# Optimization experiments

Hardware: AMD Instinct MI355X
Metric: run time of the kernel (lower is better)

The kernel has to match this reference:

```python
import jax, jax.numpy as jnp
import numpy as np

VOCAB, D, H, NC = 32000, 300, 300, 3
B, S, A, L = 256, 128, 8, 32


def _lstm_dir(x, mask, Wih, Whh, bih, bhh):
    # x: [B,T,D], mask: [B,T] bool. Returns [B,T,H] with padded steps zeroed (like pad_packed_sequence).
    Bn = x.shape[0]
    Hn = Whh.shape[1]

    def step(carry, inp):
        h, c = carry
        xt, mt = inp
        g = xt @ Wih.T + h @ Whh.T + bih + bhh  # [B,4H]
        i, f, gg, o = jnp.split(g, 4, axis=-1)
        i = jax.nn.sigmoid(i)
        f = jax.nn.sigmoid(f)
        o = jax.nn.sigmoid(o)
        cn = f * c + i * jnp.tanh(gg)
        hn = o * jnp.tanh(cn)
        m = mt[:, None]
        h2 = jnp.where(m, hn, h)
        c2 = jnp.where(m, cn, c)
        return (h2, c2), h2 * m

    init = (jnp.zeros((Bn, Hn), x.dtype), jnp.zeros((Bn, Hn), x.dtype))
    _, outs = jax.lax.scan(step, init, (jnp.swapaxes(x, 0, 1), jnp.swapaxes(mask, 0, 1)))
    return jnp.swapaxes(outs, 0, 1)


def _bilstm(x, lengths, Wih_f, Whh_f, bih_f, bhh_f, Wih_b, Whh_b, bih_b, bhh_b):
    # Emulates packed bidirectional LSTM: backward dir runs over the length-aware reversed sequence.
    Tn = x.shape[1]
    t = jnp.arange(Tn)
    mask = t[None, :] < lengths[:, None]
    out_f = _lstm_dir(x, mask, Wih_f, Whh_f, bih_f, bhh_f)
    idx = jnp.clip(lengths[:, None] - 1 - t[None, :], 0, Tn - 1)  # reversal within valid length
    x_rev = jnp.take_along_axis(x, idx[:, :, None], axis=1)
    ob = _lstm_dir(x_rev, mask, Wih_b, Whh_b, bih_b, bhh_b)
    out_b = jnp.take_along_axis(ob, idx[:, :, None], axis=1) * mask[:, :, None]
    return jnp.concatenate([out_f, out_b], axis=-1)  # [B,T,2H]


def setup_inputs() -> dict:
    key = jax.random.key(0)
    ks = jax.random.split(key, 16)
    sc = 0.05
    inp = {
        'text': jax.random.randint(ks[0], (B, S), 1, VOCAB, dtype=jnp.int32),
        'aspect': jax.random.randint(ks[1], (B, A), 1, VOCAB, dtype=jnp.int32),
        'left': jax.random.randint(ks[2], (B, L), 1, VOCAB, dtype=jnp.int32),
        'embedding': jax.random.normal(ks[3], (VOCAB, D), jnp.float32) * sc,
        'Wih_f': jax.random.normal(ks[4], (4 * H, D), jnp.float32) * sc,
        'Whh_f': jax.random.normal(ks[5], (4 * H, H), jnp.float32) * sc,
        'bih_f': jnp.zeros((4 * H,), jnp.float32),
        'bhh_f': jnp.zeros((4 * H,), jnp.float32),
        'Wih_b': jax.random.normal(ks[6], (4 * H, D), jnp.float32) * sc,
        'Whh_b': jax.random.normal(ks[7], (4 * H, H), jnp.float32) * sc,
        'bih_b': jnp.zeros((4 * H,), jnp.float32),
        'bhh_b': jnp.zeros((4 * H,), jnp.float32),
        'w1': jax.random.normal(ks[8], (2 * H, 2 * H), jnp.float32) * sc,
        'w2': jax.random.normal(ks[9], (2 * H, 2 * H), jnp.float32) * sc,
        'fc1_w': jax.random.normal(ks[10], (6 * H,), jnp.float32) * sc,
        'fc1_b': jnp.zeros((), jnp.float32),
        'fc2_w': jax.random.normal(ks[11], (NC, 8 * H), jnp.float32) * sc,
        'fc2_b': jnp.zeros((NC,), jnp.float32),
    }
    return inp


def reference(text, aspect, left, embedding, Wih_f, Whh_f, bih_f, bhh_f,
              Wih_b, Whh_b, bih_b, bhh_b, w1, w2, fc1_w, fc1_b, fc2_w, fc2_b):
    left_len = jnp.sum(left != 0, axis=-1)
    context_len = jnp.sum(text != 0, axis=-1)
    aspect_len = jnp.sum(aspect != 0, axis=-1)

    ctx = embedding[text]  # [B,S,D]
    ctx = _bilstm(ctx, context_len, Wih_f, Whh_f, bih_f, bhh_f, Wih_b, Whh_b, bih_b, bhh_b)  # [B,S,2H]

    # location weighting (locationed_context)
    t = jnp.arange(ctx.shape[1])[None, :].astype(jnp.float32)
    cl = context_len[:, None].astype(jnp.float32)
    ll = left_len[:, None].astype(jnp.float32)
    al = aspect_len[:, None].astype(jnp.float32)
    denom = cl - al + 1.0
    w = jnp.where(t < ll, 1.0 - (ll - t) / denom,
        jnp.where(t < ll + al, 0.0,
        jnp.where(t < cl, 1.0 - (t - ll - al + 1.0) / denom, 0.0)))
    ctx = ctx * w[:, :, None]

    asp = embedding[aspect]  # [B,A,D]
    asp = _bilstm(asp, aspect_len, Wih_f, Whh_f, bih_f, bhh_f, Wih_b, Whh_b, bih_b, bhh_b)  # [B,A,2H]

    # coarse aspect->context
    a_avg = jnp.sum(asp, axis=1) / aspect_len.astype(jnp.float32)[:, None]  # [B,2H]
    s1 = a_avg @ w1
    alpha1 = jax.nn.softmax(jnp.einsum('bd,bsd->bs', s1, ctx), axis=-1)
    mca = jnp.einsum('bs,bsd->bd', alpha1, ctx)

    # coarse context->aspect
    c_avg = jnp.sum(ctx, axis=1) / context_len.astype(jnp.float32)[:, None]
    s2 = c_avg @ w2
    alpha2 = jax.nn.softmax(jnp.einsum('bd,bad->ba', s2, asp), axis=-1)
    mcc = jnp.einsum('ba,bad->bd', alpha2, asp)

    # fine-grained pairwise scores: u[b,s,a] = fc1(cat(ctx_s, asp_a, ctx_s*asp_a))
    # decomposed so the [B,S,A,6H] concat tensor is never materialized
    H2 = ctx.shape[-1]
    wc, wa, wm = fc1_w[:H2], fc1_w[H2:2 * H2], fc1_w[2 * H2:]
    u = (jnp.einsum('bsd,d->bs', ctx, wc)[:, :, None]
         + jnp.einsum('bad,d->ba', asp, wa)[:, None, :]
         + jnp.einsum('bsd,bad->bsa', ctx * wm, asp)
         + fc1_b)  # [B,S,A]

    # fine aspect->context: max over aspect dim, softmax over context positions
    mfa_alpha = jax.nn.softmax(jnp.max(u, axis=2), axis=-1)  # [B,S]
    mfa = jnp.einsum('bs,bsd->bd', mfa_alpha, ctx)

    # fine context->aspect: softmax over aspect dim per position, average-pool over positions
    mfc = jnp.mean(jnp.einsum('bsa,bad->bsd', jax.nn.softmax(u, axis=-1), asp), axis=1)

    m = jnp.concatenate([mca, mcc, mfa, mfc], axis=-1)  # [B,8H]
    return jax.nn.softmax(m @ fc2_w.T + fc2_b, axis=-1)  # [B,NC]
```

## Files before the change

kernel.cpp:

```cpp
#include <hip/hip_runtime.h>
#include <hip/hip_bf16.h>
#include <hip/hip_fp16.h>


#define NB   256
#define NS   128
#define NA   8
#define NL   32
#define ND   300
#define NH   300
#define NPAD  2432
#define TOK_CTX 32768
#define PD    1216
#define HCH   20
#define HSL   4096

typedef _Float16 half8 __attribute__((ext_vector_type(8)));
typedef float    f32x4 __attribute__((ext_vector_type(4)));

__global__ void k_lengths(const int* __restrict__ text, const int* __restrict__ aspect,
                          const int* __restrict__ left, int* __restrict__ lens) {
  int b = threadIdx.x;
  if (b >= NB) return;
  int ll = 0; for (int i = 0; i < NL; i++) ll += (left[b*NL + i] != 0);
  int cl = 0; for (int i = 0; i < NS; i++) cl += (text[b*NS + i] != 0);
  int al = 0; for (int i = 0; i < NA; i++) al += (aspect[b*NA + i] != 0);
  lens[b] = ll; lens[NB + b] = cl; lens[2*NB + b] = al;
}

__global__ void k_cvt_w(const float* __restrict__ Wih_f, const float* __restrict__ Wih_b,
                        const float* __restrict__ Whh_f, const float* __restrict__ Whh_b,
                        const float* __restrict__ bih_f, const float* __restrict__ bhh_f,
                        const float* __restrict__ bih_b, const float* __restrict__ bhh_b,
                        _Float16* __restrict__ Wih_frag, _Float16* __restrict__ Whh_frag,
                        float* __restrict__ bias_sum) {
  int y = blockIdx.y;
  if (y < 2) {
    const float* sf = y ? Whh_f : Wih_f;
    const float* sb = y ? Whh_b : Wih_b;
    _Float16* dst = y ? Whh_frag : Wih_frag;
    const long N = (long)152*10*512;
    for (long i = (long)blockIdx.x*blockDim.x + threadIdx.x; i < N; i += (long)gridDim.x*blockDim.x) {
      long q = i >> 9; int r512 = (int)(i & 511);
      int l = r512 >> 3, e = r512 & 7;
      int k0 = (int)(q % 10);
      int ntile = (int)(q / 10);
      int n = ntile*16 + (l & 15);
      int k = k0*32 + (l >> 4)*8 + e;
      int d = n / PD; int rem = n - d*PD;
      int g = rem / 304; int jj = rem - g*304;
      float v = 0.f;
      if (jj < NH && k < NH) {
        const float* src = d ? sb : sf;
        v = src[(long)(g*NH + jj)*NH + k];
      }
      dst[i] = (_Float16)v;
    }
  } else {
    for (int i = blockIdx.x*blockDim.x + threadIdx.x; i < NPAD; i += gridDim.x*blockDim.x) {
      int d = i / PD; int rem = i - d*PD;
      int g = rem / 304; int jj = rem - g*304;
      float v = 0.f;
      if (jj < NH) {
        v = d ? (bih_b[g*NH + jj] + bhh_b[g*NH + jj]) : (bih_f[g*NH + jj] + bhh_f[g*NH + jj]);
      }
      bias_sum[i] = v;
    }
  }
}

__global__ __launch_bounds__(256) void k_inproj(
    const float* __restrict__ emb, const int* __restrict__ text, const int* __restrict__ aspect,
    const _Float16* __restrict__ Wih_frag, const float* __restrict__ bias_sum,
    const int* __restrict__ lens,
    _Float16* __restrict__ Pc, _Float16* __restrict__ Pa)
{
  const int l = threadIdx.x & 63, w = threadIdx.x >> 6;
  const int m0 = blockIdx.x * 128, n0 = blockIdx.y * 128;
  const int lrow = l & 15, lk = (l >> 4) * 8;
  __shared__ __align__(16) _Float16 Cs[128*136];

  const float* ap[2];
  #pragma unroll
  for (int q = 0; q < 2; q++) {
    int r = m0 + (2*w + q)*16 + lrow;
    int tok;
    if (r < TOK_CTX) { int t = r >> 8, b = r & 255; tok = text[b*NS + t]; }
    else { int rr = r - TOK_CTX; int t = rr >> 8, b = rr & 255; tok = aspect[b*NA + t]; }
    ap[q] = emb + (long)tok*ND;
  }
  const _Float16* bp = Wih_frag + (size_t)(n0 >> 4)*10*512 + l*8;

  f32x4 acc[2][8];
  #pragma unroll
  for (int q = 0; q < 2; q++)
    #pragma unroll
    for (int nt = 0; nt < 8; nt++) acc[q][nt] = (f32x4){0.f,0.f,0.f,0.f};

  #pragma unroll
  for (int k0 = 0; k0 < 9; k0++) {
    float4 f00 = *(const float4*)(ap[0] + k0*32 + lk);
    float4 f01 = *(const float4*)(ap[0] + k0*32 + lk + 4);
    float4 f10 = *(const float4*)(ap[1] + k0*32 + lk);
    float4 f11 = *(const float4*)(ap[1] + k0*32 + lk + 4);
    half8 a0, a1;
    a0[0]=(_Float16)f00.x; a0[1]=(_Float16)f00.y; a0[2]=(_Float16)f00.z; a0[3]=(_Float16)f00.w;
    a0[4]=(_Float16)f01.x; a0[5]=(_Float16)f01.y; a0[6]=(_Float16)f01.z; a0[7]=(_Float16)f01.w;
    a1[0]=(_Float16)f10.x; a1[1]=(_Float16)f10.y; a1[2]=(_Float16)f10.z; a1[3]=(_Float16)f10.w;
    a1[4]=(_Float16)f11.x; a1[5]=(_Float16)f11.y; a1[6]=(_Float16)f11.z; a1[7]=(_Float16)f11.w;
    #pragma unroll
    for (int nt = 0; nt < 8; nt++) {
      half8 bb = *(const half8*)(bp + (size_t)(nt*10 + k0)*512);
      acc[0][nt] = __builtin_amdgcn_mfma_f32_16x16x32_f16(a0, bb, acc[0][nt], 0, 0, 0);
      acc[1][nt] = __builtin_amdgcn_mfma_f32_16x16x32_f16(a1, bb, acc[1][nt], 0, 0, 0);
    }
  }
  {
    half8 a0, a1;
    #pragma unroll
    for (int j = 0; j < 8; j++) {
      int k = 288 + lk + j;
      a0[j] = (k < ND) ? (_Float16)ap[0][k] : (_Float16)0.f;
      a1[j] = (k < ND) ? (_Float16)ap[1][k] : (_Float16)0.f;
    }
    #pragma unroll
    for (int nt = 0; nt < 8; nt++) {
      half8 bb = *(const half8*)(bp + (size_t)(nt*10 + 9)*512);
      acc[0][nt] = __builtin_amdgcn_mfma_f32_16x16x32_f16(a0, bb, acc[0][nt], 0, 0, 0);
      acc[1][nt] = __builtin_amdgcn_mfma_f32_16x16x32_f16(a1, bb, acc[1][nt], 0, 0, 0);
    }
  }

  #pragma unroll
  for (int nt = 0; nt < 8; nt++) {
    float bias = bias_sum[n0 + nt*16 + lrow];
    #pragma unroll
    for (int q = 0; q < 2; q++) {
      int lr = (2*w + q)*16 + (l>>4)*4;
      #pragma unroll
      for (int r = 0; r < 4; r++)
        Cs[(lr + r)*136 + nt*16 + lrow] = (_Float16)(acc[q][nt][r] + bias);
    }
  }
  __syncthreads();

  const bool isCtx = (m0 < TOK_CTX);
  _Float16* __restrict__ Pdst = isCtx ? Pc : Pa;
  const int T2 = isCtx ? NS : NA;
  const int mrel = isCtx ? m0 : (m0 - TOK_CTX);
  const int tq = mrel >> 8;
  const int b_base = mrel & 255;
  const int lenoff = isCtx ? NB : 2*NB;
  const int chunk = l & 15;
  const int col = n0 + chunk*8;
  const int d = (col >= PD) ? 1 : 0;
  const int rem = col - d*PD;
  #pragma unroll
  for (int it = 0; it < 8; it++) {
    const int row = w*32 + it*4 + (l >> 4);
    const int b = b_base + row;
    int tp = tq; bool doit = true;
    if (d == 1) {
      int len = lens[lenoff + b];
      if (tq < len) tp = len - 1 - tq; else doit = false;
    }
    if (doit) {
      half8 v = *(const half8*)&Cs[row*136 + chunk*8];
      *(half8*)&Pdst[((size_t)(d*T2 + tp)*256 + b)*PD + rem] = v;
    }
  }
}

__global__ __launch_bounds__(256) void k_lstm_scan(
    const _Float16* __restrict__ Pc, const _Float16* __restrict__ Pa,
    const _Float16* __restrict__ Whh_frag, const int* __restrict__ lens,
    _Float16* __restrict__ hpadC, _Float16* __restrict__ hpadA,
    int* __restrict__ flags)
{
  const int lin = blockIdx.x;
  const int xcd = lin & 7;
  const int kk2 = lin >> 3;
  const int half = kk2 / 19;
  const int js = kk2 - half*19;
  const int g  = xcd + 8*half;
  const int which = g >> 3;
  const int d  = (g >> 2) & 1;
  const int mg = g & 3;

  const int l = threadIdx.x & 63, w = threadIdx.x >> 6;
  const int T = which ? NA : NS;
  const _Float16* __restrict__ Pbase = which ? Pa : Pc;
  const int* __restrict__ lenp = lens + (which ? 2*NB : NB);
  _Float16* __restrict__ hpad = which ? hpadA : hpadC;
  int* __restrict__ flg = flags + g*128;

  const int lrow = l & 15, lk = (l >> 4)*8, mrow = l >> 4;
  const int b0 = mg*64 + w*16;
  const int cbase = lk >> 4;
  const int koff  = lk & 8;

  half8 wf[10][4];
  #pragma unroll
  for (int k0 = 0; k0 < 10; k0++)
    #pragma unroll
    for (int gg = 0; gg < 4; gg++)
      wf[k0][gg] = *(const half8*)(Whh_frag +
          ((((size_t)(d*4 + gg)*19 + js)*10 + k0) << 9) + l*8);

  float cst[4];
  int   lenv[4];
  #pragma unroll
  for (int r = 0; r < 4; r++) { cst[r] = 0.f; lenv[r] = lenp[b0 + mrow*4 + r]; }

  for (int t = 0; t < T; t++) {
    const size_t slab = (size_t)(d*T + t)*256;
    float pre[4][4];
    #pragma unroll
    for (int r = 0; r < 4; r++) {
      const int b = b0 + mrow*4 + r;
      const _Float16* Pr = Pbase + (slab + b)*PD + js*16 + lrow;
      pre[r][0] = (float)Pr[0];
      pre[r][1] = (float)Pr[304];
      pre[r][2] = (float)Pr[608];
      pre[r][3] = (float)Pr[912];
    }

    f32x4 accA[4], accB[4];
    #pragma unroll
    for (int gg = 0; gg < 4; gg++) {
      accA[gg] = (f32x4){0.f,0.f,0.f,0.f};
      accB[gg] = (f32x4){0.f,0.f,0.f,0.f};
    }
    float hp[4] = {0.f, 0.f, 0.f, 0.f};

    if (t > 0) {
      if (threadIdx.x == 0) {
        int* fp = &flg[t-1];
        while (__hip_atomic_load(fp, __ATOMIC_RELAXED, __HIP_MEMORY_SCOPE_AGENT) < 19)
          __builtin_amdgcn_s_sleep(1);
      }
      __syncthreads();
      const _Float16* __restrict__ hprev = hpad + (size_t)((t-1)*2 + d)*HCH*HSL;
      #pragma unroll
      for (int r = 0; r < 4; r++)
        hp[r] = (float)hprev[(size_t)js*HSL + (b0 + mrow*4 + r)*16 + lrow];
      const _Float16* hb = hprev + (size_t)(b0 + lrow)*16 + koff;
      #pragma unroll
      for (int k0 = 0; k0 < 10; k0 += 2) {
        half8 aE = *(const half8*)(hb + (size_t)(2*k0 + cbase)*HSL);
        half8 aO = *(const half8*)(hb + (size_t)(2*(k0+1) + cbase)*HSL);
        #pragma unroll
        for (int gg = 0; gg < 4; gg++) {
          accA[gg] = __builtin_amdgcn_mfma_f32_16x16x32_f16(aE, wf[k0][gg],   accA[gg], 0, 0, 0);
          accB[gg] = __builtin_amdgcn_mfma_f32_16x16x32_f16(aO, wf[k0+1][gg], accB[gg], 0, 0, 0);
        }
      }
    }

    _Float16* __restrict__ hw = hpad + (size_t)(t*2 + d)*HCH*HSL + (size_t)js*HSL;
    #pragma unroll
    for (int r = 0; r < 4; r++) {
      const int b = b0 + mrow*4 + r;
      float gi = (accA[0][r] + accB[0][r]) + pre[r][0];
      float gf = (accA[1][r] + accB[1][r]) + pre[r][1];
      float gg2 = (accA[2][r] + accB[2][r]) + pre[r][2];
      float go = (accA[3][r] + accB[3][r]) + pre[r][3];
      float si = 1.f/(1.f + __expf(-gi));
      float sf = 1.f/(1.f + __expf(-gf));
      float so = 1.f/(1.f + __expf(-go));
      float cn = sf*cst[r] + si*tanhf(gg2);
      float hn = so*tanhf(cn);
      bool mt = t < lenv[r];
      float h2 = mt ? hn : hp[r];
      cst[r] = mt ? cn : cst[r];
      hw[(size_t)b*16 + lrow] = (_Float16)h2;
    }

    __syncthreads();
    if (threadIdx.x == 0)
      __hip_atomic_fetch_add(&flg[t], 1,
                             __ATOMIC_RELAXED, __HIP_MEMORY_SCOPE_AGENT);
  }
}

__global__ __launch_bounds__(256) void k_ctx_fused(
    const _Float16* __restrict__ hpadC, const int* __restrict__ lens,
    _Float16* __restrict__ ctx, _Float16* __restrict__ ctxT)
{
  const int b = blockIdx.x, tid = threadIdx.x;
  __shared__ float wgt_s[128];
  __shared__ int   tbv[128];
  __shared__ _Float16 tl[128][62];
  const int cl = lens[NB + b];
  if (tid < 128) {
    const int ll = lens[b], al = lens[2*NB + b];
    float clf = (float)cl, llf = (float)ll, alf = (float)al, tf = (float)tid;
    float denom = clf - alf + 1.f;
    float wgt = (tf < llf) ? (1.f - (llf - tf)/denom)
              : (tf < llf + alf) ? 0.f
              : (tf < clf) ? (1.f - (tf - llf - alf + 1.f)/denom) : 0.f;
    wgt_s[tid] = wgt;
    int tb0 = cl - 1 - tid; tbv[tid] = tb0 < 0 ? 0 : (tb0 > NS-1 ? NS-1 : tb0);
  }
  __syncthreads();
  for (int c10 = 0; c10 < 10; c10++) {
    const int j0 = c10*60;
    for (int idx = tid; idx < 128*60; idx += 256) {
      int s = idx / 60, jc = idx - s*60;
      int j = j0 + jc;
      float v;
      if (j < NH) {
        int c = j >> 4, ww = j & 15;
        v = (float)hpadC[(((size_t)(s*2 + 0)*HCH + c)*256 + b)*16 + ww];
      } else {
        int j2 = j - NH; int c = j2 >> 4, ww = j2 & 15;
        v = (float)hpadC[(((size_t)(tbv[s]*2 + 1)*HCH + c)*256 + b)*16 + ww];
      }
      v *= wgt_s[s];
      tl[s][jc] = (_Float16)v;
      ctx[((size_t)b*NS + s)*600 + j] = (_Float16)v;
    }
    __syncthreads();
    for (int idx = tid; idx < 60*128; idx += 256) {
      int jc = idx >> 7, s = idx & 127;
      ctxT[((size_t)b*600 + j0 + jc)*NS + s] = tl[s][jc];
    }
    __syncthreads();
  }
}

__global__ __launch_bounds__(320) void k_combine_asp(
    const _Float16* __restrict__ hpadA, const int* __restrict__ lens, _Float16* __restrict__ aspc)
{
  int b = blockIdx.x, tid = threadIdx.x;
  if (tid >= NH) return;
  int al = lens[2*NB + b];
  const int c = tid >> 4, ww = tid & 15;
  for (int a = 0; a < NA; a++) {
    float vf = (a < al) ? (float)hpadA[(((size_t)(a*2 + 0)*HCH + c)*256 + b)*16 + ww] : 0.f;
    int tb0 = al - 1 - a; int tb = tb0 < 0 ? 0 : (tb0 > NA-1 ? NA-1 : tb0);
    float vb = (a < al) ? (float)hpadA[(((size_t)(tb*2 + 1)*HCH + c)*256 + b)*16 + ww] : 0.f;
    aspc[((size_t)b*NA + a)*600 + tid]      = (_Float16)vf;
    aspc[((size_t)b*NA + a)*600 + NH + tid] = (_Float16)vb;
  }
}

__global__ void k_avg(const _Float16* __restrict__ ctx, const _Float16* __restrict__ aspc,
                      const int* __restrict__ lens, float* __restrict__ c_avg, float* __restrict__ a_avg) {
  int b = blockIdx.x, j = threadIdx.x;
  if (j >= 600) return;
  float ac = 0.f;
  for (int s = 0; s < NS; s++) ac += (float)ctx[((long)b*NS + s)*600 + j];
  c_avg[(long)b*600 + j] = ac / (float)lens[NB + b];
  float aa = 0.f;
  for (int a = 0; a < NA; a++) aa += (float)aspc[((long)b*NA + a)*600 + j];
  a_avg[(long)b*600 + j] = aa / (float)lens[2*NB + b];
}

__global__ void k_sw(const float* __restrict__ a_avg, const float* __restrict__ c_avg,
                     const float* __restrict__ w1, const float* __restrict__ w2,
                     float* __restrict__ s1, float* __restrict__ s2) {
  __shared__ float src[8][600];
  int bg = blockIdx.x * 8, which = blockIdx.y, tid = threadIdx.x;
  const float* sp = which ? c_avg : a_avg;
  const float* w  = which ? w2 : w1;
  float* outp     = which ? s2 : s1;
  for (int u = tid; u < 8*600; u += 640) {
    int q = u / 600, dd = u - q*600;
    src[q][dd] = sp[(long)(bg + q)*600 + dd];
  }
  __syncthreads();
  int j = tid;
  if (j >= 600) return;
  float acc[8] = {0,0,0,0,0,0,0,0};
  for (int dd = 0; dd < 600; dd++) {
    float wvv = w[dd*600 + j];
    #pragma unroll
    for (int q = 0; q < 8; q++) acc[q] += src[q][dd] * wvv;
  }
  #pragma unroll
  for (int q = 0; q < 8; q++) outp[(long)(bg + q)*600 + j] = acc[q];
}

__global__ __launch_bounds__(128) void k_att_ctx(const _Float16* __restrict__ ctxT,
    const _Float16* __restrict__ ctx, const float* __restrict__ s1, float* __restrict__ mca) {
  int b = blockIdx.x, tid = threadIdx.x;
  __shared__ float sv[600];
  __shared__ float red[128];
  __shared__ float mx, sm;
  for (int u = tid; u < 600; u += 128) sv[u] = s1[(long)b*600 + u];
  __syncthreads();
  float sc = 0.f;
  for (int dd = 0; dd < 600; dd++) sc += sv[dd] * (float)ctxT[((long)b*600 + dd)*NS + tid];
  red[tid] = sc; __syncthreads();
  if (tid == 0) { float m = -1e30f; for (int i = 0; i < 128; i++) m = fmaxf(m, red[i]); mx = m; }
  __syncthreads();
  float e = __expf(sc - mx);
  red[tid] = e; __syncthreads();
  if (tid == 0) { float s = 0.f; for (int i = 0; i < 128; i++) s += red[i]; sm = s; }
  __syncthreads();
  float alpha = e / sm;
  red[tid] = alpha; __syncthreads();
  for (int i = 0; i < 5; i++) {
    int j = tid + i*128;
    if (j < 600) {
      float acc = 0.f;
      for (int s2 = 0; s2 < NS; s2++) acc += red[s2] * (float)ctx[((long)b*NS + s2)*600 + j];
      mca[(long)b*600 + j] = acc;
    }
  }
}

__global__ void k_att_asp(const _Float16* __restrict__ aspc, const float* __restrict__ s2,
                          float* __restrict__ mcc) {
  int b = blockIdx.x, tid = threadIdx.x, wvv = tid >> 6, lane = tid & 63;
  __shared__ float sv[600];
  __shared__ float sc8[8];
  for (int u = tid; u < 600; u += 512) sv[u] = s2[(long)b*600 + u];
  __syncthreads();
  float p = 0.f;
  for (int dd = lane; dd < 600; dd += 64) p += sv[dd] * (float)aspc[((long)b*NA + wvv)*600 + dd];
  #pragma unroll
  for (int off = 32; off; off >>= 1) p += __shfl_down(p, off);
  if (lane == 0) sc8[wvv] = p;
  __syncthreads();
  float m = -1e30f;
  #pragma unroll
  for (int a = 0; a < 8; a++) m = fmaxf(m, sc8[a]);
  float es[8]; float ssum = 0.f;
  #pragma unroll
  for (int a = 0; a < 8; a++) { es[a] = __expf(sc8[a] - m); ssum += es[a]; }
  float inv = 1.f / ssum;
  for (int i = 0; i < 2; i++) {
    int j = tid + i*512;
    if (j < 600) {
      float acc = 0.f;
      #pragma unroll
      for (int a = 0; a < 8; a++) acc += es[a]*inv * (float)aspc[((long)b*NA + a)*600 + j];
      mcc[(long)b*600 + j] = acc;
    }
  }
}

__global__ __launch_bounds__(128) void k_u(const _Float16* __restrict__ ctxT, const _Float16* __restrict__ ctx,
    const _Float16* __restrict__ aspc, const float* __restrict__ fc1_w, const float* __restrict__ fc1_b,
    float* __restrict__ mfa, float* __restrict__ mfc) {
  int b = blockIdx.x, tid = threadIdx.x;
  __shared__ __align__(16) float aspl[4800];
  __shared__ float ua8[8];
  __shared__ float red[128];
  __shared__ float qa8[8];
  __shared__ float mx1, sm1;
  __shared__ float pal[128][8];
  for (int u = tid; u < 4800; u += 128) {
    int a = u / 600, dd = u - a*600;
    aspl[dd*8 + a] = (float)aspc[((long)b*NA + a)*600 + dd];
  }
  __syncthreads();
  const float* wc = fc1_w;
  const float* wa = fc1_w + 600;
  const float* wm = fc1_w + 1200;
  {
    int wvv = tid >> 6, lane = tid & 63;
    for (int q = 0; q < 4; q++) {
      int a = wvv*4 + q;
      float p = 0.f;
      for (int dd = lane; dd < 600; dd += 64) p += wa[dd] * aspl[dd*8 + a];
      #pragma unroll
      for (int off = 32; off; off >>= 1) p += __shfl_down(p, off);
      if (lane == 0) ua8[a] = p;
    }
  }
  __syncthreads();
  float x8[8] = {0,0,0,0,0,0,0,0};
  float uc = 0.f;
  for (int dd = 0; dd < 600; dd++) {
    float cv = (float)ctxT[((long)b*600 + dd)*NS + tid];
    uc += cv * wc[dd];
    float cm = cv * wm[dd];
    float4 a03 = *(const float4*)&aspl[dd*8];
    float4 a47 = *(const float4*)&aspl[dd*8 + 4];
    x8[0] += cm*a03.x; x8[1] += cm*a03.y; x8[2] += cm*a03.z; x8[3] += cm*a03.w;
    x8[4] += cm*a47.x; x8[5] += cm*a47.y; x8[6] += cm*a47.z; x8[7] += cm*a47.w;
  }
  float fb = fc1_b[0];
  float u8v[8]; float umax = -1e30f;
  #pragma unroll
  for (int a = 0; a < 8; a++) { u8v[a] = uc + ua8[a] + x8[a] + fb; umax = fmaxf(umax, u8v[a]); }
  float pa[8]; float psum = 0.f;
  #pragma unroll
  for (int a = 0; a < 8; a++) { pa[a] = __expf(u8v[a] - umax); psum += pa[a]; }
  float pin = 1.f / psum;
  #pragma unroll
  for (int a = 0; a < 8; a++) pal[tid][a] = pa[a] * pin;
  red[tid] = umax;
  __syncthreads();
  if (tid == 0) { float m = -1e30f; for (int i = 0; i < 128; i++) m = fmaxf(m, red[i]); mx1 = m; }
  if (tid < 8) { float s = 0.f; for (int i = 0; i < 128; i++) s += pal[i][tid]; qa8[tid] = s * (1.f/128.f); }
  __syncthreads();
  float e = __expf(umax - mx1);
  red[tid] = e;
  __syncthreads();
  if (tid == 0) { float s = 0.f; for (int i = 0; i < 128; i++) s += red[i]; sm1 = s; }
  __syncthreads();
  float alpha = e / sm1;
  red[tid] = alpha;
  __syncthreads();
  for (int i = 0; i < 5; i++) {
    int j = tid + i*128;
    if (j < 600) {
      float am = 0.f;
      for (int s2 = 0; s2 < NS; s2++) am += red[s2] * (float)ctx[((long)b*NS + s2)*600 + j];
      float4 a03 = *(const float4*)&aspl[j*8];
      float4 a47 = *(const float4*)&aspl[j*8 + 4];
      mfa[(long)b*600 + j] = am;
      mfc[(long)b*600 + j] = qa8[0]*a03.x + qa8[1]*a03.y + qa8[2]*a03.z + qa8[3]*a03.w
                           + qa8[4]*a47.x + qa8[5]*a47.y + qa8[6]*a47.z + qa8[7]*a47.w;
    }
  }
}

__global__ void k_final(const float* __restrict__ mca, const float* __restrict__ mcc,
                        const float* __restrict__ mfa, const float* __restrict__ mfc,
                        const float* __restrict__ fc2_w, const float* __restrict__ fc2_b,
                        float* __restrict__ out) {
  int b = blockIdx.x, tid = threadIdx.x, c = tid >> 6, lane = tid & 63;
  __shared__ float lg[3];
  float p = 0.f;
  for (int u = lane; u < 2400; u += 64) {
    int piece = u / 600;
    int jj = u - piece*600;
    const float* src = (piece == 0) ? mca : (piece == 1) ? mcc : (piece == 2) ? mfa : mfc;
    p += src[(long)b*600 + jj] * fc2_w[c*2400 + u];
  }
  #pragma unroll
  for (int off = 32; off; off >>= 1) p += __shfl_down(p, off);
  if (lane == 0) lg[c] = p + fc2_b[c];
  __syncthreads();
  if (tid == 0) {
    float m = fmaxf(lg[0], fmaxf(lg[1], lg[2]));
    float e0 = __expf(lg[0]-m), e1 = __expf(lg[1]-m), e2 = __expf(lg[2]-m);
    float s = e0 + e1 + e2;
    out[b*3 + 0] = e0/s; out[b*3 + 1] = e1/s; out[b*3 + 2] = e2/s;
  }
}

extern "C" void kernel_launch(void* const* d_in, const int* in_sizes, int n_in,
                              void* d_out, int out_size, void* d_ws, size_t ws_size,
                              hipStream_t stream)
{
  const int*   text    = (const int*)d_in[0];
  const int*   aspect  = (const int*)d_in[1];
  const int*   left    = (const int*)d_in[2];
  const float* emb     = (const float*)d_in[3];
  const float* Wih_f   = (const float*)d_in[4];
  const float* Whh_f   = (const float*)d_in[5];
  const float* bih_f   = (const float*)d_in[6];
  const float* bhh_f   = (const float*)d_in[7];
  const float* Wih_b   = (const float*)d_in[8];
  const float* Whh_b   = (const float*)d_in[9];
  const float* bih_b   = (const float*)d_in[10];
  const float* bhh_b   = (const float*)d_in[11];
  const float* w1      = (const float*)d_in[12];
  const float* w2      = (const float*)d_in[13];
  const float* fc1_w   = (const float*)d_in[14];
  const float* fc1_b   = (const float*)d_in[15];
  const float* fc2_w   = (const float*)d_in[16];
  const float* fc2_b   = (const float*)d_in[17];
  float* out = (float*)d_out;

  char* base = (char*)d_ws;
  size_t off = 0;
  auto alloc = [&](size_t bytes) -> void* {
    void* p = base + off;
    off = (off + bytes + 255) & ~(size_t)255;
    return p;
  };
  int*      lens     = (int*)     alloc(3 * NB * sizeof(int));
  int*      flags    = (int*)     alloc((size_t)16*128 * sizeof(int));
  float*    bias_sum = (float*)   alloc(NPAD * sizeof(float));
  _Float16* Wih_frag = (_Float16*)alloc((size_t)152*10*512 * sizeof(_Float16));
  _Float16* Whh_frag = (_Float16*)alloc((size_t)152*10*512 * sizeof(_Float16));
  float*    c_avg    = (float*)   alloc((size_t)NB*600 * sizeof(float));
  float*    a_avg    = (float*)   alloc((size_t)NB*600 * sizeof(float));
  float*    s1       = (float*)   alloc((size_t)NB*600 * sizeof(float));
  float*    s2       = (float*)   alloc((size_t)NB*600 * sizeof(float));
  float*    mca      = (float*)   alloc((size_t)NB*600 * sizeof(float));
  float*    mcc      = (float*)   alloc((size_t)NB*600 * sizeof(float));
  float*    mfa      = (float*)   alloc((size_t)NB*600 * sizeof(float));
  float*    mfc      = (float*)   alloc((size_t)NB*600 * sizeof(float));
  _Float16* hpadC    = (_Float16*)alloc((size_t)NS*2*HCH*HSL * sizeof(_Float16));
  _Float16* hpadA    = (_Float16*)alloc((size_t)NA*2*HCH*HSL * sizeof(_Float16));
  _Float16* Pc = (_Float16*)alloc((size_t)2*NS*NB*PD * sizeof(_Float16));
  _Float16* Pa = (_Float16*)alloc((size_t)2*NA*NB*PD * sizeof(_Float16));
  _Float16* ctx  = Pc;
  _Float16* ctxT = ctx  + (size_t)NB*NS*600;
  _Float16* aspc = ctxT + (size_t)NB*NS*600;
  if (ws_size < off) return;

  k_lengths<<<1, 256, 0, stream>>>(text, aspect, left, lens);
  k_cvt_w<<<dim3(512, 3), 256, 0, stream>>>(Wih_f, Wih_b, Whh_f, Whh_b,
                                            bih_f, bhh_f, bih_b, bhh_b,
                                            Wih_frag, Whh_frag, bias_sum);
  k_inproj<<<dim3(272, 19), 256, 0, stream>>>(emb, text, aspect, Wih_frag, bias_sum,
                                              lens, Pc, Pa);

  hipMemsetAsync(flags, 0, (size_t)16*128 * sizeof(int), stream);
  k_lstm_scan<<<304, 256, 0, stream>>>(Pc, Pa, Whh_frag, lens, hpadC, hpadA, flags);

  k_ctx_fused<<<256, 256, 0, stream>>>(hpadC, lens, ctx, ctxT);
  k_combine_asp<<<256, 320, 0, stream>>>(hpadA, lens, aspc);
  k_avg<<<256, 640, 0, stream>>>(ctx, aspc, lens, c_avg, a_avg);
  k_sw<<<dim3(32, 2), 640, 0, stream>>>(a_avg, c_avg, w1, w2, s1, s2);
  k_att_ctx<<<256, 128, 0, stream>>>(ctxT, ctx, s1, mca);
  k_att_asp<<<256, 512, 0, stream>>>(aspc, s2, mcc);
  k_u<<<256, 128, 0, stream>>>(ctxT, ctx, aspc, fc1_w, fc1_b, mfa, mfc);
  k_final<<<256, 192, 0, stream>>>(mca, mcc, mfa, mfc, fc2_w, fc2_b, out);
}
```

Baseline: 1.110 ms.

## Pre-convert embeddings to fp16, fuse averaging, per-wave scan wait, fast tanh

Adds a pass that converts the full embedding table to padded fp16 (in the hpadC buffer before the scan uses it), so the input projection loads half8 fragments directly instead of converting fp32 and handling a ragged tail. The context and aspect averages are now computed inside the combine kernels and the separate averaging kernel is removed. In the LSTM scan each wave now spins on the flag itself instead of one thread plus a block barrier, and tanhf is replaced by an exp-based tanh. Converting the whole 32000-row table costs extra bandwidth up front, the exp-based tanh can lose precision for large inputs, and the per-wave spin raises atomic polling traffic.

New measurement: 1.077 ms (median of 2 runs). 3.0% less time.

```diff
diff --git a/kernel.cpp b/kernel.cpp
--- a/kernel.cpp
+++ b/kernel.cpp
@@ -10,6 +10,7 @@
 #define ND   300
 #define NH   300
 #define NPAD  2432
+#define KP    320
 #define TOK_CTX 32768
 #define PD    1216
 #define HCH   20
@@ -17,6 +18,11 @@
 
 typedef _Float16 half8 __attribute__((ext_vector_type(8)));
 typedef float    f32x4 __attribute__((ext_vector_type(4)));
+
+__device__ __forceinline__ float fast_tanh(float x) {
+  float e = __expf(-2.f * x);
+  return 2.f / (1.f + e) - 1.f;
+}
 
 __global__ void k_lengths(const int* __restrict__ text, const int* __restrict__ aspect,
                           const int* __restrict__ left, int* __restrict__ lens) {
@@ -26,6 +32,14 @@
   int cl = 0; for (int i = 0; i < NS; i++) cl += (text[b*NS + i] != 0);
   int al = 0; for (int i = 0; i < NA; i++) al += (aspect[b*NA + i] != 0);
   lens[b] = ll; lens[NB + b] = cl; lens[2*NB + b] = al;
+}
+
+__global__ void k_cvt_emb(const float* __restrict__ emb, _Float16* __restrict__ emb16) {
+  const long N = (long)32000 * KP;
+  for (long i = (long)blockIdx.x*blockDim.x + threadIdx.x; i < N; i += (long)gridDim.x*blockDim.x) {
+    long v = i / KP; int k = (int)(i - v*KP);
+    emb16[i] = (k < ND) ? (_Float16)emb[v*ND + k] : (_Float16)0.f;
+  }
 }
 
 __global__ void k_cvt_w(const float* __restrict__ Wih_f, const float* __restrict__ Wih_b,
@@ -70,7 +84,7 @@
 }
 
 __global__ __launch_bounds__(256) void k_inproj(
-    const float* __restrict__ emb, const int* __restrict__ text, const int* __restrict__ aspect,
+    const _Float16* __restrict__ emb16, const int* __restrict__ text, const int* __restrict__ aspect,
     const _Float16* __restrict__ Wih_frag, const float* __restrict__ bias_sum,
     const int* __restrict__ lens,
     _Float16* __restrict__ Pc, _Float16* __restrict__ Pa)
@@ -80,14 +94,14 @@
   const int lrow = l & 15, lk = (l >> 4) * 8;
   __shared__ __align__(16) _Float16 Cs[128*136];
 
-  const float* ap[2];
+  const _Float16* ap[2];
   #pragma unroll
   for (int q = 0; q < 2; q++) {
     int r = m0 + (2*w + q)*16 + lrow;
     int tok;
     if (r < TOK_CTX) { int t = r >> 8, b = r & 255; tok = text[b*NS + t]; }
     else { int rr = r - TOK_CTX; int t = rr >> 8, b = rr & 255; tok = aspect[b*NA + t]; }
-    ap[q] = emb + (long)tok*ND;
+    ap[q] = emb16 + (long)tok*KP + lk;
   }
   const _Float16* bp = Wih_frag + (size_t)(n0 >> 4)*10*512 + l*8;
 
@@ -98,34 +112,12 @@
     for (int nt = 0; nt < 8; nt++) acc[q][nt] = (f32x4){0.f,0.f,0.f,0.f};
 
   #pragma unroll
-  for (int k0 = 0; k0 < 9; k0++) {
-    float4 f00 = *(const float4*)(ap[0] + k0*32 + lk);
-    float4 f01 = *(const float4*)(ap[0] + k0*32 + lk + 4);
-    float4 f10 = *(const float4*)(ap[1] + k0*32 + lk);
-    float4 f11 = *(const float4*)(ap[1] + k0*32 + lk + 4);
-    half8 a0, a1;
-    a0[0]=(_Float16)f00.x; a0[1]=(_Float16)f00.y; a0[2]=(_Float16)f00.z; a0[3]=(_Float16)f00.w;
-    a0[4]=(_Float16)f01.x; a0[5]=(_Float16)f01.y; a0[6]=(_Float16)f01.z; a0[7]=(_Float16)f01.w;
-    a1[0]=(_Float16)f10.x; a1[1]=(_Float16)f10.y; a1[2]=(_Float16)f10.z; a1[3]=(_Float16)f10.w;
-    a1[4]=(_Float16)f11.x; a1[5]=(_Float16)f11.y; a1[6]=(_Float16)f11.z; a1[7]=(_Float16)f11.w;
+  for (int k0 = 0; k0 < 10; k0++) {
+    half8 a0 = *(const half8*)(ap[0] + k0*32);
+    half8 a1 = *(const half8*)(ap[1] + k0*32);
     #pragma unroll
     for (int nt = 0; nt < 8; nt++) {
       half8 bb = *(const half8*)(bp + (size_t)(nt*10 + k0)*512);
-      acc[0][nt] = __builtin_amdgcn_mfma_f32_16x16x32_f16(a0, bb, acc[0][nt], 0, 0, 0);
-      acc[1][nt] = __builtin_amdgcn_mfma_f32_16x16x32_f16(a1, bb, acc[1][nt], 0, 0, 0);
-    }
-  }
-  {
-    half8 a0, a1;
-    #pragma unroll
-    for (int j = 0; j < 8; j++) {
-      int k = 288 + lk + j;
-      a0[j] = (k < ND) ? (_Float16)ap[0][k] : (_Float16)0.f;
-      a1[j] = (k < ND) ? (_Float16)ap[1][k] : (_Float16)0.f;
-    }
-    #pragma unroll
-    for (int nt = 0; nt < 8; nt++) {
-      half8 bb = *(const half8*)(bp + (size_t)(nt*10 + 9)*512);
       acc[0][nt] = __builtin_amdgcn_mfma_f32_16x16x32_f16(a0, bb, acc[0][nt], 0, 0, 0);
       acc[1][nt] = __builtin_amdgcn_mfma_f32_16x16x32_f16(a1, bb, acc[1][nt], 0, 0, 0);
     }
@@ -234,12 +226,11 @@
     float hp[4] = {0.f, 0.f, 0.f, 0.f};
 
     if (t > 0) {
-      if (threadIdx.x == 0) {
+      if (l == 0) {
         int* fp = &flg[t-1];
         while (__hip_atomic_load(fp, __ATOMIC_RELAXED, __HIP_MEMORY_SCOPE_AGENT) < 19)
           __builtin_amdgcn_s_sleep(1);
       }
-      __syncthreads();
       const _Float16* __restrict__ hprev = hpad + (size_t)((t-1)*2 + d)*HCH*HSL;
       #pragma unroll
       for (int r = 0; r < 4; r++)
@@ -268,8 +259,8 @@
       float si = 1.f/(1.f + __expf(-gi));
       float sf = 1.f/(1.f + __expf(-gf));
       float so = 1.f/(1.f + __expf(-go));
-      float cn = sf*cst[r] + si*tanhf(gg2);
-      float hn = so*tanhf(cn);
+      float cn = sf*cst[r] + si*fast_tanh(gg2);
+      float hn = so*fast_tanh(cn);
       bool mt = t < lenv[r];
       float h2 = mt ? hn : hp[r];
       cst[r] = mt ? cn : cst[r];
@@ -285,7 +276,7 @@
 
 __global__ __launch_bounds__(256) void k_ctx_fused(
     const _Float16* __restrict__ hpadC, const int* __restrict__ lens,
-    _Float16* __restrict__ ctx, _Float16* __restrict__ ctxT)
+    _Float16* __restrict__ ctx, _Float16* __restrict__ ctxT, float* __restrict__ c_avg)
 {
   const int b = blockIdx.x, tid = threadIdx.x;
   __shared__ float wgt_s[128];
@@ -303,6 +294,7 @@
     int tb0 = cl - 1 - tid; tbv[tid] = tb0 < 0 ? 0 : (tb0 > NS-1 ? NS-1 : tb0);
   }
   __syncthreads();
+  const float clinv = 1.f / (float)cl;
   for (int c10 = 0; c10 < 10; c10++) {
     const int j0 = c10*60;
     for (int idx = tid; idx < 128*60; idx += 256) {
@@ -325,36 +317,35 @@
       int jc = idx >> 7, s = idx & 127;
       ctxT[((size_t)b*600 + j0 + jc)*NS + s] = tl[s][jc];
     }
+    if (tid < 60) {
+      float sum = 0.f;
+      for (int s = 0; s < 128; s++) sum += (float)tl[s][tid];
+      c_avg[(size_t)b*600 + j0 + tid] = sum * clinv;
+    }
     __syncthreads();
   }
 }
 
 __global__ __launch_bounds__(320) void k_combine_asp(
-    const _Float16* __restrict__ hpadA, const int* __restrict__ lens, _Float16* __restrict__ aspc)
+    const _Float16* __restrict__ hpadA, const int* __restrict__ lens,
+    _Float16* __restrict__ aspc, float* __restrict__ a_avg)
 {
   int b = blockIdx.x, tid = threadIdx.x;
   if (tid >= NH) return;
   int al = lens[2*NB + b];
+  const float alinv = 1.f / (float)al;
   const int c = tid >> 4, ww = tid & 15;
+  float sumF = 0.f, sumB = 0.f;
   for (int a = 0; a < NA; a++) {
     float vf = (a < al) ? (float)hpadA[(((size_t)(a*2 + 0)*HCH + c)*256 + b)*16 + ww] : 0.f;
     int tb0 = al - 1 - a; int tb = tb0 < 0 ? 0 : (tb0 > NA-1 ? NA-1 : tb0);
     float vb = (a < al) ? (float)hpadA[(((size_t)(tb*2 + 1)*HCH + c)*256 + b)*16 + ww] : 0.f;
     aspc[((size_t)b*NA + a)*600 + tid]      = (_Float16)vf;
     aspc[((size_t)b*NA + a)*600 + NH + tid] = (_Float16)vb;
-  }
-}
-
-__global__ void k_avg(const _Float16* __restrict__ ctx, const _Float16* __restrict__ aspc,
-                      const int* __restrict__ lens, float* __restrict__ c_avg, float* __restrict__ a_avg) {
-  int b = blockIdx.x, j = threadIdx.x;
-  if (j >= 600) return;
-  float ac = 0.f;
-  for (int s = 0; s < NS; s++) ac += (float)ctx[((long)b*NS + s)*600 + j];
-  c_avg[(long)b*600 + j] = ac / (float)lens[NB + b];
-  float aa = 0.f;
-  for (int a = 0; a < NA; a++) aa += (float)aspc[((long)b*NA + a)*600 + j];
-  a_avg[(long)b*600 + j] = aa / (float)lens[2*NB + b];
+    sumF += vf; sumB += vb;
+  }
+  a_avg[(size_t)b*600 + tid]      = sumF * alinv;
+  a_avg[(size_t)b*600 + NH + tid] = sumB * alinv;
 }
 
 __global__ void k_sw(const float* __restrict__ a_avg, const float* __restrict__ c_avg,
@@ -591,6 +582,7 @@
   float*    mfc      = (float*)   alloc((size_t)NB*600 * sizeof(float));
   _Float16* hpadC    = (_Float16*)alloc((size_t)NS*2*HCH*HSL * sizeof(_Float16));
   _Float16* hpadA    = (_Float16*)alloc((size_t)NA*2*HCH*HSL * sizeof(_Float16));
+  _Float16* emb16    = hpadC;
   _Float16* Pc = (_Float16*)alloc((size_t)2*NS*NB*PD * sizeof(_Float16));
   _Float16* Pa = (_Float16*)alloc((size_t)2*NA*NB*PD * sizeof(_Float16));
   _Float16* ctx  = Pc;
@@ -599,18 +591,18 @@
   if (ws_size < off) return;
 
   k_lengths<<<1, 256, 0, stream>>>(text, aspect, left, lens);
+  k_cvt_emb<<<2048, 256, 0, stream>>>(emb, emb16);
   k_cvt_w<<<dim3(512, 3), 256, 0, stream>>>(Wih_f, Wih_b, Whh_f, Whh_b,
                                             bih_f, bhh_f, bih_b, bhh_b,
                                             Wih_frag, Whh_frag, bias_sum);
-  k_inproj<<<dim3(272, 19), 256, 0, stream>>>(emb, text, aspect, Wih_frag, bias_sum,
+  k_inproj<<<dim3(272, 19), 256, 0, stream>>>(emb16, text, aspect, Wih_frag, bias_sum,
                                               lens, Pc, Pa);
 
   hipMemsetAsync(flags, 0, (size_t)16*128 * sizeof(int), stream);
   k_lstm_scan<<<304, 256, 0, stream>>>(Pc, Pa, Whh_frag, lens, hpadC, hpadA, flags);
 
-  k_ctx_fused<<<256, 256, 0, stream>>>(hpadC, lens, ctx, ctxT);
-  k_combine_asp<<<256, 320, 0, stream>>>(hpadA, lens, aspc);
-  k_avg<<<256, 640, 0, stream>>>(ctx, aspc, lens, c_avg, a_avg);
+  k_ctx_fused<<<256, 256, 0, stream>>>(hpadC, lens, ctx, ctxT, c_avg);
+  k_combine_asp<<<256, 320, 0, stream>>>(hpadA, lens, aspc, a_avg);
   k_sw<<<dim3(32, 2), 640, 0, stream>>>(a_avg, c_avg, w1, w2, s1, s2);
   k_att_ctx<<<256, 128, 0, stream>>>(ctxT, ctx, s1, mca);
   k_att_asp<<<256, 512, 0, stream>>>(aspc, s2, mcc);
```
